# Performance work log

Hardware: AMD Instinct MI355X
Metric: run time of the kernel (lower is better)

The kernel has to match this reference:

```python
import jax, jax.numpy as jnp
import numpy as np

D_MODEL = 1024
D_CODEX = 64
CODEX_SIZE = 8192
BETA = 1.0
EPS_NORM = 1e-12
EPS_LN = 1e-5


def l2norm(x):
    # F.normalize(p=2, dim=-1, eps=1e-12): x / max(||x||, eps)
    n = jnp.sqrt(jnp.sum(x * x, axis=-1, keepdims=True))
    return x / jnp.maximum(n, EPS_NORM)


def setup_inputs() -> dict:
    key = jax.random.key(0)
    ks = jax.random.split(key, 8)
    B, S = 4, 2048
    Z = jax.random.normal(ks[0], (B, S, D_MODEL), dtype=jnp.float32)
    W1 = 0.02 * jax.random.normal(ks[1], (D_MODEL, D_MODEL), dtype=jnp.float32)
    b1 = jnp.zeros((D_MODEL,), dtype=jnp.float32)
    W2 = 0.02 * jax.random.normal(ks[2], (D_MODEL, D_CODEX), dtype=jnp.float32)
    b2 = jnp.zeros((D_CODEX,), dtype=jnp.float32)
    codex = l2norm(jax.random.normal(ks[3], (CODEX_SIZE, D_CODEX), dtype=jnp.float32))
    ln_w = jnp.ones((D_CODEX,), dtype=jnp.float32)
    ln_b = jnp.zeros((D_CODEX,), dtype=jnp.float32)
    Wp = 0.02 * jax.random.normal(ks[4], (D_CODEX, D_MODEL), dtype=jnp.float32)
    bp = jnp.zeros((D_MODEL,), dtype=jnp.float32)
    return {"Z": Z, "W1": W1, "b1": b1, "W2": W2, "b2": b2,
            "codex": codex, "ln_w": ln_w, "ln_b": ln_b, "Wp": Wp, "bp": bp}


def reference(Z, W1, b1, W2, b2, codex, ln_w, ln_b, Wp, bp):
    # pre_proj: Linear -> Tanh -> Linear, then l2-normalize into codex space
    Z_e = jnp.tanh(Z @ W1 + b1) @ W2 + b2            # (B, S, d_codex)
    Z_e = l2norm(Z_e)
    flat = Z_e.reshape(-1, D_CODEX)                  # (N, d_codex)
    # squared-L2 distances: |z|^2 + |c|^2 - 2 z.c
    dists = (jnp.sum(flat * flat, axis=-1, keepdims=True)
             + jnp.sum(codex * codex, axis=-1)[None, :]
             - 2.0 * jnp.einsum('nd,cd->nc', flat, codex))  # (N, K)
    idxs = jnp.argmin(dists, axis=-1).reshape(Z_e.shape[:-1])  # (B, S)
    codex_probs = jax.nn.one_hot(idxs, CODEX_SIZE, dtype=Z_e.dtype)  # (B, S, K)
    Z_q = codex[idxs]                                 # (B, S, d_codex)
    # commitment loss (codex is an EMA buffer, no gradient through it)
    loss = BETA * jnp.mean((jax.lax.stop_gradient(Z_q) - Z_e) ** 2)
    # straight-through estimator
    Z_q = Z_e + jax.lax.stop_gradient(Z_q - Z_e)
    # layernorm over d_codex
    mu = jnp.mean(Z_q, axis=-1, keepdims=True)
    var = jnp.mean((Z_q - mu) ** 2, axis=-1, keepdims=True)
    Z_q = (Z_q - mu) * jax.lax.rsqrt(var + EPS_LN) * ln_w + ln_b
    # post_proj back to d_model
    Z_q = Z_q @ Wp + bp                               # (B, S, d_model)
    return Z_q, loss, codex_probs
```

## Files before the change

kernel.cpp:

```cpp
#include <hip/hip_runtime.h>
#include <math.h>
#include <stdint.h>

#define N_TOK   8192
#define DMODEL  1024
#define DCODEX  64
#define KCODES  8192

typedef short short8 __attribute__((ext_vector_type(8)));
typedef float f32x16 __attribute__((ext_vector_type(16)));

union Frag { short8 s; uint2 u[2]; };

__device__ __forceinline__ unsigned short f2bf(float f) {
    unsigned u = __float_as_uint(f);
    unsigned r = u + 0x7FFFu + ((u >> 16) & 1u);
    return (unsigned short)(r >> 16);
}
__device__ __forceinline__ float bf2f(unsigned short h) {
    return __uint_as_float(((unsigned)h) << 16);
}

__global__ __launch_bounds__(256) void codenorm_kernel(const float* __restrict__ codex,
                                                       float* __restrict__ cn2) {
    int k = blockIdx.x * 256 + threadIdx.x;
    const float4* p = (const float4*)(codex + (size_t)k * DCODEX);
    float s = 0.f;
#pragma unroll
    for (int i = 0; i < 16; ++i) {
        float4 v = p[i];
        s += v.x * v.x + v.y * v.y + v.z * v.z + v.w * v.w;
    }
    cn2[k] = s;
}

__global__ __launch_bounds__(256) void split3_kernel(const float* __restrict__ src,
                                                     unsigned short* __restrict__ p0,
                                                     unsigned short* __restrict__ p1,
                                                     unsigned short* __restrict__ p2) {
    size_t i4 = ((size_t)blockIdx.x * 256 + threadIdx.x) * 4;
    float4 v = *(const float4*)(src + i4);
    float f[4] = {v.x, v.y, v.z, v.w};
    ushort4 h0, h1, h2;
#pragma unroll
    for (int c = 0; c < 4; ++c) {
        unsigned short a0 = f2bf(f[c]);
        float r1 = f[c] - bf2f(a0);
        unsigned short a1 = f2bf(r1);
        float r2 = r1 - bf2f(a1);
        unsigned short a2 = f2bf(r2);
        ((unsigned short*)&h0)[c] = a0;
        ((unsigned short*)&h1)[c] = a1;
        ((unsigned short*)&h2)[c] = a2;
    }
    *(ushort4*)(p0 + i4) = h0;
    *(ushort4*)(p1 + i4) = h1;
    *(ushort4*)(p2 + i4) = h2;
}

__global__ __launch_bounds__(256) void split_w1_kernel(const float* __restrict__ W1,
                                                       unsigned short* __restrict__ t0,
                                                       unsigned short* __restrict__ t1,
                                                       unsigned short* __restrict__ t2) {
    __shared__ float tile[32][33];
    const int tid = threadIdx.x;
    const int k0 = blockIdx.x * 32;
    const int n0 = blockIdx.y * 32;
    {
        int i = tid >> 3, j4 = (tid & 7) * 4;
        float4 v = *(const float4*)(W1 + (size_t)(k0 + i) * DMODEL + n0 + j4);
        tile[i][j4 + 0] = v.x; tile[i][j4 + 1] = v.y;
        tile[i][j4 + 2] = v.z; tile[i][j4 + 3] = v.w;
    }
    __syncthreads();
    int n = tid >> 3, kq = (tid & 7) * 4;
    ushort4 h0, h1, h2;
#pragma unroll
    for (int c = 0; c < 4; ++c) {
        float f = tile[kq + c][n];
        unsigned short a0 = f2bf(f);
        float r1 = f - bf2f(a0);
        unsigned short a1 = f2bf(r1);
        float r2 = r1 - bf2f(a1);
        unsigned short a2 = f2bf(r2);
        ((unsigned short*)&h0)[c] = a0;
        ((unsigned short*)&h1)[c] = a1;
        ((unsigned short*)&h2)[c] = a2;
    }
    size_t off = (size_t)(n0 + n) * DMODEL + k0 + kq;
    *(ushort4*)(t0 + off) = h0;
    *(ushort4*)(t1 + off) = h1;
    *(ushort4*)(t2 + off) = h2;
}

__global__ __launch_bounds__(256) void gemm1_mfma_kernel(const unsigned short* __restrict__ Zt0,
                                                         const unsigned short* __restrict__ Zt1,
                                                         const unsigned short* __restrict__ Zt2,
                                                         const unsigned short* __restrict__ W1t0,
                                                         const unsigned short* __restrict__ W1t1,
                                                         const unsigned short* __restrict__ W1t2,
                                                         const float* __restrict__ b1,
                                                         float* __restrict__ H) {
    __shared__ unsigned short Ash[3][128][36];
    __shared__ unsigned short Bsh[3][128][36];
    const int tid = threadIdx.x;
    const int row0 = blockIdx.x * 128;
    const int col0 = blockIdx.y * 128;
    const int wave = tid >> 6;
    const int lane = tid & 63;
    const int lrow = lane & 31;
    const int lhalf = lane >> 5;
    const int wm = wave >> 1, wn = wave & 1;

    const unsigned short* Ap[3] = {Zt0, Zt1, Zt2};
    const unsigned short* Bp[3] = {W1t0, W1t1, W1t2};

    f32x16 acc[2][2];
#pragma unroll
    for (int i = 0; i < 2; ++i)
#pragma unroll
        for (int j = 0; j < 2; ++j)
#pragma unroll
            for (int r = 0; r < 16; ++r) acc[i][j][r] = 0.f;

    for (int k0 = 0; k0 < DMODEL; k0 += 32) {
        __syncthreads();
#pragma unroll
        for (int l = 0; l < 3; ++l) {
#pragma unroll
            for (int t = 0; t < 2; ++t) {
                int q = tid + t * 256;
                int r = q >> 2, kq = (q & 3) * 8;
                uint4 va = *(const uint4*)(Ap[l] + (size_t)(row0 + r) * DMODEL + k0 + kq);
                *(uint2*)&Ash[l][r][kq]     = make_uint2(va.x, va.y);
                *(uint2*)&Ash[l][r][kq + 4] = make_uint2(va.z, va.w);
                uint4 vb = *(const uint4*)(Bp[l] + (size_t)(col0 + r) * DMODEL + k0 + kq);
                *(uint2*)&Bsh[l][r][kq]     = make_uint2(vb.x, vb.y);
                *(uint2*)&Bsh[l][r][kq + 4] = make_uint2(vb.z, vb.w);
            }
        }
        __syncthreads();
#pragma unroll
        for (int mk = 0; mk < 2; ++mk) {
            const int kb = mk * 16 + lhalf * 8;
            Frag ah[2], am[2], al[2], bh[2], bm[2], bl[2];
#pragma unroll
            for (int ti = 0; ti < 2; ++ti) {
                int rA = wm * 64 + ti * 32 + lrow;
                ah[ti].u[0] = *(const uint2*)&Ash[0][rA][kb];
                ah[ti].u[1] = *(const uint2*)&Ash[0][rA][kb + 4];
                am[ti].u[0] = *(const uint2*)&Ash[1][rA][kb];
                am[ti].u[1] = *(const uint2*)&Ash[1][rA][kb + 4];
                al[ti].u[0] = *(const uint2*)&Ash[2][rA][kb];
                al[ti].u[1] = *(const uint2*)&Ash[2][rA][kb + 4];
            }
#pragma unroll
            for (int tj = 0; tj < 2; ++tj) {
                int rB = wn * 64 + tj * 32 + lrow;
                bh[tj].u[0] = *(const uint2*)&Bsh[0][rB][kb];
                bh[tj].u[1] = *(const uint2*)&Bsh[0][rB][kb + 4];
                bm[tj].u[0] = *(const uint2*)&Bsh[1][rB][kb];
                bm[tj].u[1] = *(const uint2*)&Bsh[1][rB][kb + 4];
                bl[tj].u[0] = *(const uint2*)&Bsh[2][rB][kb];
                bl[tj].u[1] = *(const uint2*)&Bsh[2][rB][kb + 4];
            }
#pragma unroll
            for (int ti = 0; ti < 2; ++ti)
#pragma unroll
                for (int tj = 0; tj < 2; ++tj) {
                    acc[ti][tj] = __builtin_amdgcn_mfma_f32_32x32x16_bf16(ah[ti].s, bh[tj].s, acc[ti][tj], 0, 0, 0);
                    acc[ti][tj] = __builtin_amdgcn_mfma_f32_32x32x16_bf16(ah[ti].s, bm[tj].s, acc[ti][tj], 0, 0, 0);
                    acc[ti][tj] = __builtin_amdgcn_mfma_f32_32x32x16_bf16(am[ti].s, bh[tj].s, acc[ti][tj], 0, 0, 0);
                    acc[ti][tj] = __builtin_amdgcn_mfma_f32_32x32x16_bf16(am[ti].s, bm[tj].s, acc[ti][tj], 0, 0, 0);
                    acc[ti][tj] = __builtin_amdgcn_mfma_f32_32x32x16_bf16(ah[ti].s, bl[tj].s, acc[ti][tj], 0, 0, 0);
                    acc[ti][tj] = __builtin_amdgcn_mfma_f32_32x32x16_bf16(al[ti].s, bh[tj].s, acc[ti][tj], 0, 0, 0);
                }
        }
    }

    float b1v[2];
#pragma unroll
    for (int tj = 0; tj < 2; ++tj) b1v[tj] = b1[col0 + wn * 64 + tj * 32 + lrow];
#pragma unroll
    for (int ti = 0; ti < 2; ++ti)
#pragma unroll
        for (int tj = 0; tj < 2; ++tj) {
            int col = col0 + wn * 64 + tj * 32 + lrow;
#pragma unroll
            for (int r = 0; r < 16; ++r) {
                int row = row0 + wm * 64 + ti * 32 + (r & 3) + 8 * (r >> 2) + 4 * lhalf;
                H[(size_t)row * DMODEL + col] = tanhf(acc[ti][tj][r] + b1v[tj]);
            }
        }
}

__global__ __launch_bounds__(256) void gemm2_norm_kernel(const float* __restrict__ H,
                                                         const float* __restrict__ W2,
                                                         const float* __restrict__ b2,
                                                         float* __restrict__ Ze) {
    __shared__ float As[64][36];
    __shared__ float Bs[64][68];
    const int tid = threadIdx.x;
    const int row0 = blockIdx.x * 32;
    const int ty = tid >> 4, tx = tid & 15;

    float acc[2][4];
#pragma unroll
    for (int i = 0; i < 2; ++i)
#pragma unroll
        for (int j = 0; j < 4; ++j) acc[i][j] = 0.f;

    for (int k0 = 0; k0 < DMODEL; k0 += 64) {
        __syncthreads();
#pragma unroll
        for (int t = 0; t < 2; ++t) {
            int q = tid + t * 256;
            int r = q >> 4, k4 = (q & 15) * 4;
            float4 v = *(const float4*)(H + (size_t)(row0 + r) * DMODEL + k0 + k4);
            As[k4 + 0][r] = v.x; As[k4 + 1][r] = v.y;
            As[k4 + 2][r] = v.z; As[k4 + 3][r] = v.w;
        }
#pragma unroll
        for (int t = 0; t < 4; ++t) {
            int q = tid + t * 256;
            int kk = q >> 4, c4 = (q & 15) * 4;
            *(float4*)&Bs[kk][c4] = *(const float4*)(W2 + (size_t)(k0 + kk) * DCODEX + c4);
        }
        __syncthreads();
#pragma unroll
        for (int k = 0; k < 64; ++k) {
            float2 a = *(const float2*)&As[k][ty * 2];
            float4 b = *(const float4*)&Bs[k][tx * 4];
            float bw[4] = {b.x, b.y, b.z, b.w};
#pragma unroll
            for (int j = 0; j < 4; ++j) {
                acc[0][j] = fmaf(a.x, bw[j], acc[0][j]);
                acc[1][j] = fmaf(a.y, bw[j], acc[1][j]);
            }
        }
    }
    float4 b2v4 = *(const float4*)(b2 + tx * 4);
    float b2v[4] = {b2v4.x, b2v4.y, b2v4.z, b2v4.w};
#pragma unroll
    for (int i = 0; i < 2; ++i) {
        float e[4];
#pragma unroll
        for (int j = 0; j < 4; ++j) e[j] = acc[i][j] + b2v[j];
        float ss = e[0] * e[0] + e[1] * e[1] + e[2] * e[2] + e[3] * e[3];
        ss += __shfl_xor(ss, 8, 64);
        ss += __shfl_xor(ss, 4, 64);
        ss += __shfl_xor(ss, 2, 64);
        ss += __shfl_xor(ss, 1, 64);
        float nrm = fmaxf(sqrtf(ss), 1e-12f);
        float o[4];
#pragma unroll
        for (int j = 0; j < 4; ++j) o[j] = e[j] / nrm;
        *(float4*)(Ze + (size_t)(row0 + ty * 2 + i) * DCODEX + tx * 4) = *(float4*)&o[0];
    }
}

__device__ __forceinline__ unsigned fenc(float f) {
    unsigned u = __float_as_uint(f);
    return (u & 0x80000000u) ? ~u : (u | 0x80000000u);
}
__device__ __forceinline__ unsigned long long ullmin2(unsigned long long a,
                                                      unsigned long long b) {
    return a < b ? a : b;
}

__global__ __launch_bounds__(256) void dist_mfma_kernel(const unsigned short* __restrict__ Zh,
                                                        const unsigned short* __restrict__ Zm,
                                                        const unsigned short* __restrict__ Zl,
                                                        const unsigned short* __restrict__ Ch,
                                                        const unsigned short* __restrict__ Cm,
                                                        const unsigned short* __restrict__ Cl,
                                                        const float* __restrict__ cn2,
                                                        unsigned long long* __restrict__ gbest) {
    __shared__ unsigned short Ash[3][128][36];
    __shared__ unsigned short Bsh[3][128][36];
    __shared__ unsigned long long red[128];
    const int tid = threadIdx.x;
    const int row0 = blockIdx.x * 128;
    const int col0 = blockIdx.y * 128;
    const int wave = tid >> 6;
    const int lane = tid & 63;
    const int lrow = lane & 31;
    const int lhalf = lane >> 5;
    const int wm = wave >> 1, wn = wave & 1;

    const unsigned short* Ap[3] = {Zh, Zm, Zl};
    const unsigned short* Bp[3] = {Ch, Cm, Cl};

    if (tid < 128) red[tid] = 0xFFFFFFFFFFFFFFFFull;

    f32x16 acc[2][2];
#pragma unroll
    for (int i = 0; i < 2; ++i)
#pragma unroll
        for (int j = 0; j < 2; ++j)
#pragma unroll
            for (int r = 0; r < 16; ++r) acc[i][j][r] = 0.f;

#pragma unroll
    for (int k0 = 0; k0 < DCODEX; k0 += 32) {
        __syncthreads();
#pragma unroll
        for (int l = 0; l < 3; ++l) {
#pragma unroll
            for (int t = 0; t < 2; ++t) {
                int q = tid + t * 256;
                int r = q >> 2, kq = (q & 3) * 8;
                uint4 va = *(const uint4*)(Ap[l] + (size_t)(row0 + r) * DCODEX + k0 + kq);
                *(uint2*)&Ash[l][r][kq]     = make_uint2(va.x, va.y);
                *(uint2*)&Ash[l][r][kq + 4] = make_uint2(va.z, va.w);
                uint4 vb = *(const uint4*)(Bp[l] + (size_t)(col0 + r) * DCODEX + k0 + kq);
                *(uint2*)&Bsh[l][r][kq]     = make_uint2(vb.x, vb.y);
                *(uint2*)&Bsh[l][r][kq + 4] = make_uint2(vb.z, vb.w);
            }
        }
        __syncthreads();
#pragma unroll
        for (int mk = 0; mk < 2; ++mk) {
            const int kb = mk * 16 + lhalf * 8;
            Frag ah[2], am[2], al[2], bh[2], bm[2], bl[2];
#pragma unroll
            for (int ti = 0; ti < 2; ++ti) {
                int rA = wm * 64 + ti * 32 + lrow;
                ah[ti].u[0] = *(const uint2*)&Ash[0][rA][kb];
                ah[ti].u[1] = *(const uint2*)&Ash[0][rA][kb + 4];
                am[ti].u[0] = *(const uint2*)&Ash[1][rA][kb];
                am[ti].u[1] = *(const uint2*)&Ash[1][rA][kb + 4];
                al[ti].u[0] = *(const uint2*)&Ash[2][rA][kb];
                al[ti].u[1] = *(const uint2*)&Ash[2][rA][kb + 4];
            }
#pragma unroll
            for (int tj = 0; tj < 2; ++tj) {
                int rB = wn * 64 + tj * 32 + lrow;
                bh[tj].u[0] = *(const uint2*)&Bsh[0][rB][kb];
                bh[tj].u[1] = *(const uint2*)&Bsh[0][rB][kb + 4];
                bm[tj].u[0] = *(const uint2*)&Bsh[1][rB][kb];
                bm[tj].u[1] = *(const uint2*)&Bsh[1][rB][kb + 4];
                bl[tj].u[0] = *(const uint2*)&Bsh[2][rB][kb];
                bl[tj].u[1] = *(const uint2*)&Bsh[2][rB][kb + 4];
            }
#pragma unroll
            for (int ti = 0; ti < 2; ++ti)
#pragma unroll
                for (int tj = 0; tj < 2; ++tj) {
                    acc[ti][tj] = __builtin_amdgcn_mfma_f32_32x32x16_bf16(ah[ti].s, bh[tj].s, acc[ti][tj], 0, 0, 0);
                    acc[ti][tj] = __builtin_amdgcn_mfma_f32_32x32x16_bf16(ah[ti].s, bm[tj].s, acc[ti][tj], 0, 0, 0);
                    acc[ti][tj] = __builtin_amdgcn_mfma_f32_32x32x16_bf16(am[ti].s, bh[tj].s, acc[ti][tj], 0, 0, 0);
                    acc[ti][tj] = __builtin_amdgcn_mfma_f32_32x32x16_bf16(am[ti].s, bm[tj].s, acc[ti][tj], 0, 0, 0);
                    acc[ti][tj] = __builtin_amdgcn_mfma_f32_32x32x16_bf16(ah[ti].s, bl[tj].s, acc[ti][tj], 0, 0, 0);
                    acc[ti][tj] = __builtin_amdgcn_mfma_f32_32x32x16_bf16(al[ti].s, bh[tj].s, acc[ti][tj], 0, 0, 0);
                }
        }
    }

    float cnv[2];
#pragma unroll
    for (int tj = 0; tj < 2; ++tj) cnv[tj] = cn2[col0 + wn * 64 + tj * 32 + lrow];
#pragma unroll
    for (int ti = 0; ti < 2; ++ti) {
#pragma unroll
        for (int r = 0; r < 16; ++r) {
            int rloc = wm * 64 + ti * 32 + (r & 3) + 8 * (r >> 2) + 4 * lhalf;
            unsigned long long kmin = 0xFFFFFFFFFFFFFFFFull;
#pragma unroll
            for (int tj = 0; tj < 2; ++tj) {
                float dist = fmaf(-2.0f, acc[ti][tj][r], cnv[tj]);
                unsigned col = (unsigned)(col0 + wn * 64 + tj * 32 + lrow);
                unsigned long long key = ((unsigned long long)fenc(dist) << 32) | col;
                kmin = ullmin2(kmin, key);
            }
#pragma unroll
            for (int m = 1; m <= 16; m <<= 1)
                kmin = ullmin2(kmin, (unsigned long long)__shfl_xor((long long)kmin, m, 64));
            if (lrow == 0) atomicMin(&red[rloc], kmin);
        }
    }
    __syncthreads();
    if (tid < 128) atomicMin(&gbest[row0 + tid], red[tid]);
}

__global__ __launch_bounds__(256) void zero_scatter_kernel(const unsigned long long* __restrict__ gbest,
                                                           float* __restrict__ probs) {
    size_t g = (size_t)blockIdx.x * 256 + threadIdx.x;
    int row = (int)(g >> 11);
    int c4i = (int)(g & 2047);
    unsigned id = (unsigned)(gbest[row] & 0xFFFFFFFFull);
    float4 v = {0.f, 0.f, 0.f, 0.f};
    if ((id >> 2) == (unsigned)c4i) ((float*)&v)[id & 3] = 1.0f;
    *(float4*)(probs + ((size_t)row << 13) + ((size_t)c4i << 2)) = v;
}

__global__ __launch_bounds__(256) void ln_loss_kernel(const unsigned long long* __restrict__ gbest,
                                                      const float* __restrict__ codex,
                                                      const float* __restrict__ Ze,
                                                      const float* __restrict__ ln_w,
                                                      const float* __restrict__ ln_b,
                                                      float* __restrict__ Aln,
                                                      float* __restrict__ loss) {
    const int tid = threadIdx.x;
    const int w = tid >> 6, l = tid & 63;
    const int row = blockIdx.x * 4 + w;
    int id = (int)(unsigned)(gbest[row] & 0xFFFFFFFFull);
    float zq = codex[(size_t)id * DCODEX + l];
    float ze = Ze[(size_t)row * DCODEX + l];
    float dlt = zq - ze;
    float val = ze + dlt;
    float s = val;
#pragma unroll
    for (int m = 32; m >= 1; m >>= 1) s += __shfl_xor(s, m, 64);
    float mu = s * 0.015625f;
    float c = val - mu;
    float v2 = c * c;
#pragma unroll
    for (int m = 32; m >= 1; m >>= 1) v2 += __shfl_xor(v2, m, 64);
    float var = v2 * 0.015625f;
    float y = c * (1.0f / sqrtf(var + 1e-5f)) * ln_w[l] + ln_b[l];
    Aln[(size_t)row * DCODEX + l] = y;
    float d2 = dlt * dlt;
#pragma unroll
    for (int m = 32; m >= 1; m >>= 1) d2 += __shfl_xor(d2, m, 64);
    if (l == 0) atomicAdd(loss, d2 * (1.0f / 524288.0f));
}

__global__ __launch_bounds__(256) void gemm3_kernel(const float* __restrict__ Aln,
                                                    const float* __restrict__ Wp,
                                                    const float* __restrict__ bp,
                                                    float* __restrict__ Zq) {
    __shared__ float As[64][132];
    __shared__ float Bs[64][68];
    const int tid = threadIdx.x;
    const int row0 = blockIdx.x * 128;
    const int col0 = blockIdx.y * 64;
    const int ty = tid >> 4, tx = tid & 15;

#pragma unroll
    for (int t = 0; t < 8; ++t) {
        int q = tid + t * 256;
        int r = q >> 4, d4 = (q & 15) * 4;
        float4 v = *(const float4*)(Aln + (size_t)(row0 + r) * DCODEX + d4);
        As[d4 + 0][r] = v.x; As[d4 + 1][r] = v.y;
        As[d4 + 2][r] = v.z; As[d4 + 3][r] = v.w;
    }
#pragma unroll
    for (int t = 0; t < 4; ++t) {
        int q = tid + t * 256;
        int kk = q >> 4, c4 = (q & 15) * 4;
        *(float4*)&Bs[kk][c4] = *(const float4*)(Wp + (size_t)kk * DMODEL + col0 + c4);
    }
    __syncthreads();

    float acc[8][4];
#pragma unroll
    for (int i = 0; i < 8; ++i)
#pragma unroll
        for (int j = 0; j < 4; ++j) acc[i][j] = 0.f;
#pragma unroll
    for (int k = 0; k < 64; ++k) {
        float a[8];
        *(float4*)&a[0] = *(const float4*)&As[k][ty * 4];
        *(float4*)&a[4] = *(const float4*)&As[k][64 + ty * 4];
        float4 b = *(const float4*)&Bs[k][tx * 4];
        float bw[4] = {b.x, b.y, b.z, b.w};
#pragma unroll
        for (int i = 0; i < 8; ++i)
#pragma unroll
            for (int j = 0; j < 4; ++j)
                acc[i][j] = fmaf(a[i], bw[j], acc[i][j]);
    }
    float4 bp4 = *(const float4*)(bp + col0 + tx * 4);
    float bb[4] = {bp4.x, bp4.y, bp4.z, bp4.w};
#pragma unroll
    for (int half = 0; half < 2; ++half)
#pragma unroll
        for (int i = 0; i < 4; ++i) {
            int r = row0 + half * 64 + ty * 4 + i;
            float o[4];
#pragma unroll
            for (int j = 0; j < 4; ++j) o[j] = acc[half * 4 + i][j] + bb[j];
            *(float4*)(Zq + (size_t)r * DMODEL + col0 + tx * 4) = *(float4*)&o[0];
        }
}

extern "C" void kernel_launch(void* const* d_in, const int* in_sizes, int n_in,
                              void* d_out, int out_size, void* d_ws, size_t ws_size,
                              hipStream_t stream) {
    const float* Z     = (const float*)d_in[0];
    const float* W1    = (const float*)d_in[1];
    const float* b1    = (const float*)d_in[2];
    const float* W2    = (const float*)d_in[3];
    const float* b2    = (const float*)d_in[4];
    const float* codex = (const float*)d_in[5];
    const float* ln_w  = (const float*)d_in[6];
    const float* ln_b  = (const float*)d_in[7];
    const float* Wp    = (const float*)d_in[8];
    const float* bp    = (const float*)d_in[9];

    float* out      = (float*)d_out;
    float* Zq_out   = out;
    float* loss_out = out + (size_t)N_TOK * DMODEL;
    float* probs    = loss_out + 1;

    char* ws = (char*)d_ws;
    float* H   = (float*)ws;
    float* Aln = H;
    float* Ze  = H + (size_t)N_TOK * DMODEL;
    float* cn2 = Ze + (size_t)N_TOK * DCODEX;
    unsigned long long* gbest = (unsigned long long*)(cn2 + KCODES);
    unsigned short* W1t0 = (unsigned short*)(gbest + N_TOK);
    unsigned short* W1t1 = W1t0 + (size_t)DMODEL * DMODEL;
    unsigned short* W1t2 = W1t1 + (size_t)DMODEL * DMODEL;
    unsigned short* Zt0  = W1t2 + (size_t)DMODEL * DMODEL;
    unsigned short* Zt1  = Zt0 + (size_t)N_TOK * DMODEL;
    unsigned short* Zt2  = Zt1 + (size_t)N_TOK * DMODEL;
    unsigned short* Zeh  = Zt2 + (size_t)N_TOK * DMODEL;
    unsigned short* Zem  = Zeh + (size_t)N_TOK * DCODEX;
    unsigned short* Zel  = Zem + (size_t)N_TOK * DCODEX;
    unsigned short* Chh  = Zel + (size_t)N_TOK * DCODEX;
    unsigned short* Chm  = Chh + (size_t)KCODES * DCODEX;
    unsigned short* Chl  = Chm + (size_t)KCODES * DCODEX;

    hipMemsetAsync(loss_out, 0, sizeof(float), stream);
    hipMemsetAsync(gbest, 0xFF, (size_t)N_TOK * sizeof(unsigned long long), stream);

    codenorm_kernel<<<KCODES / 256, 256, 0, stream>>>(codex, cn2);
    split_w1_kernel<<<dim3(DMODEL / 32, DMODEL / 32), 256, 0, stream>>>(W1, W1t0, W1t1, W1t2);
    split3_kernel<<<(int)(((size_t)N_TOK * DMODEL) / 1024), 256, 0, stream>>>(Z, Zt0, Zt1, Zt2);
    split3_kernel<<<(int)(((size_t)KCODES * DCODEX) / 1024), 256, 0, stream>>>(codex, Chh, Chm, Chl);
    gemm1_mfma_kernel<<<dim3(N_TOK / 128, DMODEL / 128), 256, 0, stream>>>(Zt0, Zt1, Zt2, W1t0, W1t1, W1t2, b1, H);
    gemm2_norm_kernel<<<N_TOK / 32, 256, 0, stream>>>(H, W2, b2, Ze);
    split3_kernel<<<(int)(((size_t)N_TOK * DCODEX) / 1024), 256, 0, stream>>>(Ze, Zeh, Zem, Zel);
    dist_mfma_kernel<<<dim3(N_TOK / 128, KCODES / 128), 256, 0, stream>>>(Zeh, Zem, Zel, Chh, Chm, Chl, cn2, gbest);
    zero_scatter_kernel<<<(int)(((size_t)N_TOK * KCODES / 4) / 256), 256, 0, stream>>>(gbest, probs);
    ln_loss_kernel<<<N_TOK / 4, 256, 0, stream>>>(gbest, codex, Ze, ln_w, ln_b, Aln, loss_out);
    gemm3_kernel<<<dim3(N_TOK / 128, DMODEL / 64), 256, 0, stream>>>(Aln, Wp, bp, Zq_out);
}
```

Baseline: 773.4 us.

## Use two-term fp16 split for distance GEMM and nontemporal one-hot stores

Replaces the three-term bf16 split (six MFMAs per tile step) in the distance kernel with a two-term fp16 hi/lo split needing three fp16 MFMAs, since fp16 carries more mantissa bits for the unit-norm vectors. The whole 64-wide K dimension is now loaded into shared memory once, which removes the K-loop barriers. The one-hot probs writes switch to nontemporal stores to avoid polluting caches. The cost is a small loss of precision in the dot products, which could flip argmin on near-ties.

```diff
diff --git a/kernel.cpp b/kernel.cpp
--- a/kernel.cpp
+++ b/kernel.cpp
@@ -8,9 +8,13 @@
 #define KCODES  8192
 
 typedef short short8 __attribute__((ext_vector_type(8)));
+typedef _Float16 half8 __attribute__((ext_vector_type(8)));
 typedef float f32x16 __attribute__((ext_vector_type(16)));
-
-union Frag { short8 s; uint2 u[2]; };
+typedef float f32x4  __attribute__((ext_vector_type(4)));
+
+union Frag  { short8 s; uint2 u[2]; };
+union FragH { half8  h; uint2 u[2]; };
+union H16   { _Float16 h; unsigned short s; };
 
 __device__ __forceinline__ unsigned short f2bf(float f) {
     unsigned u = __float_as_uint(f);
@@ -56,6 +60,26 @@
     *(ushort4*)(p0 + i4) = h0;
     *(ushort4*)(p1 + i4) = h1;
     *(ushort4*)(p2 + i4) = h2;
+}
+
+__global__ __launch_bounds__(256) void split2h_kernel(const float* __restrict__ src,
+                                                      unsigned short* __restrict__ p0,
+                                                      unsigned short* __restrict__ p1) {
+    size_t i4 = ((size_t)blockIdx.x * 256 + threadIdx.x) * 4;
+    float4 v = *(const float4*)(src + i4);
+    float f[4] = {v.x, v.y, v.z, v.w};
+    ushort4 h0, h1;
+#pragma unroll
+    for (int c = 0; c < 4; ++c) {
+        H16 a0, a1;
+        a0.h = (_Float16)f[c];
+        float r = f[c] - (float)a0.h;
+        a1.h = (_Float16)r;
+        ((unsigned short*)&h0)[c] = a0.s;
+        ((unsigned short*)&h1)[c] = a1.s;
+    }
+    *(ushort4*)(p0 + i4) = h0;
+    *(ushort4*)(p1 + i4) = h1;
 }
 
 __global__ __launch_bounds__(256) void split_w1_kernel(const float* __restrict__ W1,
@@ -270,14 +294,12 @@
 
 __global__ __launch_bounds__(256) void dist_mfma_kernel(const unsigned short* __restrict__ Zh,
                                                         const unsigned short* __restrict__ Zm,
-                                                        const unsigned short* __restrict__ Zl,
                                                         const unsigned short* __restrict__ Ch,
                                                         const unsigned short* __restrict__ Cm,
-                                                        const unsigned short* __restrict__ Cl,
                                                         const float* __restrict__ cn2,
                                                         unsigned long long* __restrict__ gbest) {
-    __shared__ unsigned short Ash[3][128][36];
-    __shared__ unsigned short Bsh[3][128][36];
+    __shared__ unsigned short Ash[2][128][68];
+    __shared__ unsigned short Bsh[2][128][68];
     __shared__ unsigned long long red[128];
     const int tid = threadIdx.x;
     const int row0 = blockIdx.x * 128;
@@ -288,11 +310,27 @@
     const int lhalf = lane >> 5;
     const int wm = wave >> 1, wn = wave & 1;
 
-    const unsigned short* Ap[3] = {Zh, Zm, Zl};
-    const unsigned short* Bp[3] = {Ch, Cm, Cl};
+    const unsigned short* Ap[2] = {Zh, Zm};
+    const unsigned short* Bp[2] = {Ch, Cm};
 
     if (tid < 128) red[tid] = 0xFFFFFFFFFFFFFFFFull;
 
+#pragma unroll
+    for (int l = 0; l < 2; ++l) {
+#pragma unroll
+        for (int t = 0; t < 4; ++t) {
+            int q = tid + t * 256;
+            int r = q >> 3, kq = (q & 7) * 8;
+            uint4 va = *(const uint4*)(Ap[l] + (size_t)(row0 + r) * DCODEX + kq);
+            *(uint2*)&Ash[l][r][kq]     = make_uint2(va.x, va.y);
+            *(uint2*)&Ash[l][r][kq + 4] = make_uint2(va.z, va.w);
+            uint4 vb = *(const uint4*)(Bp[l] + (size_t)(col0 + r) * DCODEX + kq);
+            *(uint2*)&Bsh[l][r][kq]     = make_uint2(vb.x, vb.y);
+            *(uint2*)&Bsh[l][r][kq + 4] = make_uint2(vb.z, vb.w);
+        }
+    }
+    __syncthreads();
+
     f32x16 acc[2][2];
 #pragma unroll
     for (int i = 0; i < 2; ++i)
@@ -302,59 +340,33 @@
             for (int r = 0; r < 16; ++r) acc[i][j][r] = 0.f;
 
 #pragma unroll
-    for (int k0 = 0; k0 < DCODEX; k0 += 32) {
-        __syncthreads();
-#pragma unroll
-        for (int l = 0; l < 3; ++l) {
-#pragma unroll
-            for (int t = 0; t < 2; ++t) {
-                int q = tid + t * 256;
-                int r = q >> 2, kq = (q & 3) * 8;
-                uint4 va = *(const uint4*)(Ap[l] + (size_t)(row0 + r) * DCODEX + k0 + kq);
-                *(uint2*)&Ash[l][r][kq]     = make_uint2(va.x, va.y);
-                *(uint2*)&Ash[l][r][kq + 4] = make_uint2(va.z, va.w);
-                uint4 vb = *(const uint4*)(Bp[l] + (size_t)(col0 + r) * DCODEX + k0 + kq);
-                *(uint2*)&Bsh[l][r][kq]     = make_uint2(vb.x, vb.y);
-                *(uint2*)&Bsh[l][r][kq + 4] = make_uint2(vb.z, vb.w);
-            }
-        }
-        __syncthreads();
-#pragma unroll
-        for (int mk = 0; mk < 2; ++mk) {
-            const int kb = mk * 16 + lhalf * 8;
-            Frag ah[2], am[2], al[2], bh[2], bm[2], bl[2];
-#pragma unroll
-            for (int ti = 0; ti < 2; ++ti) {
-                int rA = wm * 64 + ti * 32 + lrow;
-                ah[ti].u[0] = *(const uint2*)&Ash[0][rA][kb];
-                ah[ti].u[1] = *(const uint2*)&Ash[0][rA][kb + 4];
-                am[ti].u[0] = *(const uint2*)&Ash[1][rA][kb];
-                am[ti].u[1] = *(const uint2*)&Ash[1][rA][kb + 4];
-                al[ti].u[0] = *(const uint2*)&Ash[2][rA][kb];
-                al[ti].u[1] = *(const uint2*)&Ash[2][rA][kb + 4];
-            }
+    for (int mk = 0; mk < 4; ++mk) {
+        const int kb = mk * 16 + lhalf * 8;
+        FragH a0[2], a1[2], b0[2], b1[2];
+#pragma unroll
+        for (int ti = 0; ti < 2; ++ti) {
+            int rA = wm * 64 + ti * 32 + lrow;
+            a0[ti].u[0] = *(const uint2*)&Ash[0][rA][kb];
+            a0[ti].u[1] = *(const uint2*)&Ash[0][rA][kb + 4];
+            a1[ti].u[0] = *(const uint2*)&Ash[1][rA][kb];
+            a1[ti].u[1] = *(const uint2*)&Ash[1][rA][kb + 4];
+        }
+#pragma unroll
+        for (int tj = 0; tj < 2; ++tj) {
+            int rB = wn * 64 + tj * 32 + lrow;
+            b0[tj].u[0] = *(const uint2*)&Bsh[0][rB][kb];
+            b0[tj].u[1] = *(const uint2*)&Bsh[0][rB][kb + 4];
+            b1[tj].u[0] = *(const uint2*)&Bsh[1][rB][kb];
+            b1[tj].u[1] = *(const uint2*)&Bsh[1][rB][kb + 4];
+        }
+#pragma unroll
+        for (int ti = 0; ti < 2; ++ti)
 #pragma unroll
             for (int tj = 0; tj < 2; ++tj) {
-                int rB = wn * 64 + tj * 32 + lrow;
-                bh[tj].u[0] = *(const uint2*)&Bsh[0][rB][kb];
-                bh[tj].u[1] = *(const uint2*)&Bsh[0][rB][kb + 4];
-                bm[tj].u[0] = *(const uint2*)&Bsh[1][rB][kb];
-                bm[tj].u[1] = *(const uint2*)&Bsh[1][rB][kb + 4];
-                bl[tj].u[0] = *(const uint2*)&Bsh[2][rB][kb];
-                bl[tj].u[1] = *(const uint2*)&Bsh[2][rB][kb + 4];
-            }
-#pragma unroll
-            for (int ti = 0; ti < 2; ++ti)
-#pragma unroll
-                for (int tj = 0; tj < 2; ++tj) {
-                    acc[ti][tj] = __builtin_amdgcn_mfma_f32_32x32x16_bf16(ah[ti].s, bh[tj].s, acc[ti][tj], 0, 0, 0);
-                    acc[ti][tj] = __builtin_amdgcn_mfma_f32_32x32x16_bf16(ah[ti].s, bm[tj].s, acc[ti][tj], 0, 0, 0);
-                    acc[ti][tj] = __builtin_amdgcn_mfma_f32_32x32x16_bf16(am[ti].s, bh[tj].s, acc[ti][tj], 0, 0, 0);
-                    acc[ti][tj] = __builtin_amdgcn_mfma_f32_32x32x16_bf16(am[ti].s, bm[tj].s, acc[ti][tj], 0, 0, 0);
-                    acc[ti][tj] = __builtin_amdgcn_mfma_f32_32x32x16_bf16(ah[ti].s, bl[tj].s, acc[ti][tj], 0, 0, 0);
-                    acc[ti][tj] = __builtin_amdgcn_mfma_f32_32x32x16_bf16(al[ti].s, bh[tj].s, acc[ti][tj], 0, 0, 0);
-                }
-        }
+                acc[ti][tj] = __builtin_amdgcn_mfma_f32_32x32x16_f16(a0[ti].h, b0[tj].h, acc[ti][tj], 0, 0, 0);
+                acc[ti][tj] = __builtin_amdgcn_mfma_f32_32x32x16_f16(a0[ti].h, b1[tj].h, acc[ti][tj], 0, 0, 0);
+                acc[ti][tj] = __builtin_amdgcn_mfma_f32_32x32x16_f16(a1[ti].h, b0[tj].h, acc[ti][tj], 0, 0, 0);
+            }
     }
 
     float cnv[2];
@@ -389,9 +401,9 @@
     int row = (int)(g >> 11);
     int c4i = (int)(g & 2047);
     unsigned id = (unsigned)(gbest[row] & 0xFFFFFFFFull);
-    float4 v = {0.f, 0.f, 0.f, 0.f};
-    if ((id >> 2) == (unsigned)c4i) ((float*)&v)[id & 3] = 1.0f;
-    *(float4*)(probs + ((size_t)row << 13) + ((size_t)c4i << 2)) = v;
+    f32x4 v = {0.f, 0.f, 0.f, 0.f};
+    if ((id >> 2) == (unsigned)c4i) v[id & 3] = 1.0f;
+    __builtin_nontemporal_store(v, (f32x4*)(probs + ((size_t)row << 13) + ((size_t)c4i << 2)));
 }
 
 __global__ __launch_bounds__(256) void ln_loss_kernel(const unsigned long long* __restrict__ gbest,
@@ -518,10 +530,8 @@
     unsigned short* Zt2  = Zt1 + (size_t)N_TOK * DMODEL;
     unsigned short* Zeh  = Zt2 + (size_t)N_TOK * DMODEL;
     unsigned short* Zem  = Zeh + (size_t)N_TOK * DCODEX;
-    unsigned short* Zel  = Zem + (size_t)N_TOK * DCODEX;
-    unsigned short* Chh  = Zel + (size_t)N_TOK * DCODEX;
-    unsigned short* Chm  = Chh + (size_t)KCODES * DCODEX;
-    unsigned short* Chl  = Chm + (size_t)KCODES * DCODEX;
+    unsigned short* Cxh  = Zem + (size_t)N_TOK * DCODEX;
+    unsigned short* Cxm  = Cxh + (size_t)KCODES * DCODEX;
 
     hipMemsetAsync(loss_out, 0, sizeof(float), stream);
     hipMemsetAsync(gbest, 0xFF, (size_t)N_TOK * sizeof(unsigned long long), stream);
@@ -529,11 +539,11 @@
     codenorm_kernel<<<KCODES / 256, 256, 0, stream>>>(codex, cn2);
     split_w1_kernel<<<dim3(DMODEL / 32, DMODEL / 32), 256, 0, stream>>>(W1, W1t0, W1t1, W1t2);
     split3_kernel<<<(int)(((size_t)N_TOK * DMODEL) / 1024), 256, 0, stream>>>(Z, Zt0, Zt1, Zt2);
-    split3_kernel<<<(int)(((size_t)KCODES * DCODEX) / 1024), 256, 0, stream>>>(codex, Chh, Chm, Chl);
+    split2h_kernel<<<(int)(((size_t)KCODES * DCODEX) / 1024), 256, 0, stream>>>(codex, Cxh, Cxm);
     gemm1_mfma_kernel<<<dim3(N_TOK / 128, DMODEL / 128), 256, 0, stream>>>(Zt0, Zt1, Zt2, W1t0, W1t1, W1t2, b1, H);
     gemm2_norm_kernel<<<N_TOK / 32, 256, 0, stream>>>(H, W2, b2, Ze);
-    split3_kernel<<<(int)(((size_t)N_TOK * DCODEX) / 1024), 256, 0, stream>>>(Ze, Zeh, Zem, Zel);
-    dist_mfma_kernel<<<dim3(N_TOK / 128, KCODES / 128), 256, 0, stream>>>(Zeh, Zem, Zel, Chh, Chm, Chl, cn2, gbest);
+    split2h_kernel<<<(int)(((size_t)N_TOK * DCODEX) / 1024), 256, 0, stream>>>(Ze, Zeh, Zem);
+    dist_mfma_kernel<<<dim3(N_TOK / 128, KCODES / 128), 256, 0, stream>>>(Zeh, Zem, Cxh, Cxm, cn2, gbest);
     zero_scatter_kernel<<<(int)(((size_t)N_TOK * KCODES / 4) / 256), 256, 0, stream>>>(gbest, probs);
     ln_loss_kernel<<<N_TOK / 4, 256, 0, stream>>>(gbest, codex, Ze, ln_w, ln_b, Aln, loss_out);
     gemm3_kernel<<<dim3(N_TOK / 128, DMODEL / 64), 256, 0, stream>>>(Aln, Wp, bp, Zq_out);
```

Result: faster. 731.4 us (-5.4%).
